# Performance work log

Measured on AMD Instinct MI355X. Metric: run time of the kernel, lower is better.

The kernel has to match this reference:

```python
import jax, jax.numpy as jnp
import numpy as np

N = 50000      # nodes
E = 800000     # edges (avg degree 16)
F_IN = 256     # num_node_features
H = 256        # hidden_dim
L = 2          # num_message_passing_rounds - 1 hidden conv layers


def setup_inputs() -> dict:
    key = jax.random.key(0)
    ks = jax.random.split(key, 8)
    x = jax.random.normal(ks[0], (N, F_IN), dtype=jnp.float32)
    edge_index = jax.random.randint(ks[1], (2, E), 0, N, dtype=jnp.int32)
    init = lambda k, shape, fan: jax.random.normal(k, shape, dtype=jnp.float32) / np.float32(np.sqrt(fan))
    WA_in = init(ks[2], (F_IN, H), F_IN)   # proj_in.A weight (stored [in,out])
    WB_in = init(ks[3], (F_IN, H), F_IN)   # proj_in.B weight
    A_stack = init(ks[4], (L, H, H), H)    # conv layers' A weights
    B_stack = init(ks[5], (L, H, H), H)    # conv layers' B weights
    W_out = init(ks[6], (H, 1), H)         # proj_out weight
    b_out = jnp.zeros((1,), jnp.float32)   # proj_out bias
    return {"x": x, "edge_index": edge_index, "WA_in": WA_in, "WB_in": WB_in,
            "A_stack": A_stack, "B_stack": B_stack, "W_out": W_out, "b_out": b_out}


def reference(x, edge_index, WA_in, WB_in, A_stack, B_stack, W_out, b_out):
    src, dst = edge_index[0], edge_index[1]
    # in-degree per node; PyG scatter-mean divides by max(deg, 1)
    deg = jax.ops.segment_sum(jnp.ones((E,), x.dtype), dst, num_segments=N)
    inv_deg = (1.0 / jnp.maximum(deg, 1.0))[:, None]  # [N,1]

    def mean_agg(h):
        # gather x_j = h[src], scatter-mean into dst -> [N, d]
        return jax.ops.segment_sum(h[src], dst, num_segments=N) * inv_deg

    # proj_in: A(mean_msg) + B(x)
    h = mean_agg(x) @ WA_in + x @ WB_in
    # hidden conv rounds with sigmoid (use_relu=False)
    for i in range(L):
        h = jax.nn.sigmoid(mean_agg(h) @ A_stack[i] + h @ B_stack[i])
    # proj_out + squeeze (output_logits=True)
    return (h @ W_out + b_out).squeeze()  # [N]
```

## Files before the change

### kernel.cpp

```cpp
#include <hip/hip_runtime.h>

typedef unsigned short u16;
typedef unsigned int u32;
typedef __attribute__((ext_vector_type(8))) short short8;
typedef __attribute__((ext_vector_type(4))) float f32x4;
typedef __attribute__((ext_vector_type(2))) float f32x2;

__device__ __forceinline__ float bf2f(u16 u) {
    return __uint_as_float(((u32)u) << 16);
}
__device__ __forceinline__ u16 f2bf(float f) {
    u32 u = __float_as_uint(f);
    u += 0x7fff + ((u >> 16) & 1);
    return (u16)(u >> 16);
}
__device__ __forceinline__ u32 pack2(float a, float b) {
    return (u32)f2bf(a) | ((u32)f2bf(b) << 16);
}
__device__ __forceinline__ u32 pk_fp8x4(float f0, float f1, float f2, float f3) {
    int w = __builtin_amdgcn_cvt_pk_fp8_f32(f0, f1, 0, false);
    w = __builtin_amdgcn_cvt_pk_fp8_f32(f2, f3, w, true);
    return (u32)w;
}
__device__ __forceinline__ void acc4(float* a, u32 w) {
    f32x2 lo = __builtin_amdgcn_cvt_pk_f32_fp8((int)w, false);
    f32x2 hi = __builtin_amdgcn_cvt_pk_f32_fp8((int)w, true);
    a[0] += lo.x; a[1] += lo.y; a[2] += hi.x; a[3] += hi.y;
}
__device__ __forceinline__ void acc4m(float* a, u32 w, float m) {
    f32x2 lo = __builtin_amdgcn_cvt_pk_f32_fp8((int)w, false);
    f32x2 hi = __builtin_amdgcn_cvt_pk_f32_fp8((int)w, true);
    a[0] += m * lo.x; a[1] += m * lo.y; a[2] += m * hi.x; a[3] += m * hi.y;
}
__device__ __forceinline__ void acc16(float* a, uint4 v) {
    acc4(a + 0, v.x); acc4(a + 4, v.y); acc4(a + 8, v.z); acc4(a + 12, v.w);
}
__device__ __forceinline__ void acc16m(float* a, uint4 v, float m) {
    acc4m(a + 0, v.x, m); acc4m(a + 4, v.y, m); acc4m(a + 8, v.z, m); acc4m(a + 12, v.w, m);
}


__global__ void cvt_x_kernel(const float* __restrict__ x, u16* __restrict__ xb,
                             u32* __restrict__ xq, int n) {
    int i = blockIdx.x * 256 + threadIdx.x;
    int row = i >> 6;
    ushort4 o;
    u32 q;
    if (row < n) {
        float4 v = ((const float4*)x)[i];
        o.x = f2bf(v.x); o.y = f2bf(v.y); o.z = f2bf(v.z); o.w = f2bf(v.w);
        q = pk_fp8x4(v.x, v.y, v.z, v.w);
    } else {
        o.x = o.y = o.z = o.w = 0;
        q = 0;
    }
    ((ushort4*)xb)[i] = o;
    xq[i] = q;
}

__global__ void cvt_h_kernel(const u16* __restrict__ hb, uint2* __restrict__ hq, int ngroups) {
    int j = blockIdx.x * 256 + threadIdx.x;
    if (j >= ngroups) return;
    uint4 v = ((const uint4*)hb)[j];
    float f0 = bf2f(v.x & 0xffff), f1 = bf2f(v.x >> 16);
    float f2 = bf2f(v.y & 0xffff), f3 = bf2f(v.y >> 16);
    float f4 = bf2f(v.z & 0xffff), f5 = bf2f(v.z >> 16);
    float f6 = bf2f(v.w & 0xffff), f7 = bf2f(v.w >> 16);
    uint2 o;
    o.x = pk_fp8x4(f0, f1, f2, f3);
    o.y = pk_fp8x4(f4, f5, f6, f7);
    hq[j] = o;
}

__global__ void cvt_w_kernel(const float* __restrict__ WA, const float* __restrict__ WB,
                             const float* __restrict__ As, const float* __restrict__ Bs,
                             u16* __restrict__ wT, int nlayers) {
    int i = blockIdx.x * 256 + threadIdx.x;
    const int per = 256 * 512;
    if (i >= nlayers * per) return;
    int l = i / per;
    int rem = i - l * per;
    int nn = rem >> 9;
    int k = rem & 511;
    const float* Aw = (l == 0) ? WA : As + (size_t)(l - 1) * 65536;
    const float* Bw = (l == 0) ? WB : Bs + (size_t)(l - 1) * 65536;
    float v = (k < 256) ? Aw[(size_t)k * 256 + nn] : Bw[(size_t)(k - 256) * 256 + nn];
    wT[i] = f2bf(v);
}


__global__ void count_kernel(const int* __restrict__ dst, int* __restrict__ deg, int e) {
    int i = blockIdx.x * 256 + threadIdx.x;
    if (i < e) atomicAdd(&deg[dst[i]], 1);
}

__global__ void scan_local_kernel(const int* __restrict__ deg, int* __restrict__ rowptr,
                                  int* __restrict__ bsum, int n) {
    __shared__ int sh[256];
    int t = threadIdx.x;
    int i = blockIdx.x * 256 + t;
    int v = (i < n) ? deg[i] : 0;
    int x = v;
    sh[t] = x; __syncthreads();
    for (int o = 1; o < 256; o <<= 1) {
        int y = (t >= o) ? sh[t - o] : 0;
        __syncthreads();
        x += y; sh[t] = x; __syncthreads();
    }
    if (i < n) rowptr[i] = x - v;
    if (t == 255) bsum[blockIdx.x] = x;
}

__global__ void scan_block_kernel(const int* __restrict__ bsum, int* __restrict__ boff, int nb) {
    __shared__ int sh[256];
    int t = threadIdx.x;
    int v = (t < nb) ? bsum[t] : 0;
    int x = v;
    sh[t] = x; __syncthreads();
    for (int o = 1; o < 256; o <<= 1) {
        int y = (t >= o) ? sh[t - o] : 0;
        __syncthreads();
        x += y; sh[t] = x; __syncthreads();
    }
    if (t < nb) boff[t] = x - v;
}

__global__ void scan_add_kernel(int* __restrict__ rowptr, const int* __restrict__ boff,
                                const int* __restrict__ deg, float* __restrict__ invd,
                                int n, int e) {
    int i = blockIdx.x * 256 + threadIdx.x;
    if (i < n) {
        rowptr[i] += boff[i >> 8];
        int d = deg[i];
        invd[i] = 1.0f / (float)(d > 0 ? d : 1);
    }
    if (i == 0) rowptr[n] = e;
}

__global__ void fill_kernel(const int* __restrict__ src, const int* __restrict__ dst,
                            const int* __restrict__ rowptr, int* __restrict__ fillc,
                            int* __restrict__ srcs, int e) {
    int i = blockIdx.x * 256 + threadIdx.x;
    if (i >= e) return;
    int d = dst[i];
    int pos = rowptr[d] + atomicAdd(&fillc[d], 1);
    srcs[pos] = src[i];
}


__global__ __launch_bounds__(256) void agg_kernel(const unsigned char* __restrict__ q,
                                                  u16* __restrict__ mb,
                                                  const int* __restrict__ rowptr,
                                                  const int* __restrict__ srcs,
                                                  const float* __restrict__ invd,
                                                  int n, int npad) {
    int gw = (blockIdx.x * 256 + threadIdx.x) >> 6;
    int lane = threadIdx.x & 63;
    int qd = lane >> 4;
    int fl = lane & 15;
    if (gw >= npad) return;
    u16* orow = mb + (size_t)gw * 256;
    if (gw >= n) {
        if (lane < 16) {
            uint4 z; z.x = z.y = z.z = z.w = 0;
            uint4* p = (uint4*)(orow + lane * 16);
            p[0] = z; p[1] = z;
        }
        return;
    }
    int beg = rowptr[gw], end = rowptr[gw + 1];
    float a[16];
#pragma unroll
    for (int i = 0; i < 16; ++i) a[i] = 0.f;
    for (int base = beg; base < end; base += 64) {
        int cnt = end - base;
        if (cnt > 64) cnt = 64;
        int el = (lane < cnt) ? srcs[base + lane] : 0;
        int t = 0;
        for (; 4 * t + 8 <= cnt; t += 2) {
            int s0 = __shfl(el, 4 * t + qd);
            int s1 = __shfl(el, 4 * t + 4 + qd);
            uint4 v0 = *(const uint4*)(q + (size_t)s0 * 256 + fl * 16);
            uint4 v1 = *(const uint4*)(q + (size_t)s1 * 256 + fl * 16);
            acc16(a, v0);
            acc16(a, v1);
        }
        for (; 4 * t < cnt; ++t) {
            int ei = 4 * t + qd;
            int sj = __shfl(el, ei & 63);
            float m = (ei < cnt) ? 1.0f : 0.0f;
            uint4 v = *(const uint4*)(q + (size_t)sj * 256 + fl * 16);
            acc16m(a, v, m);
        }
    }
#pragma unroll
    for (int i = 0; i < 16; ++i) {
        a[i] += __shfl_xor(a[i], 16);
        a[i] += __shfl_xor(a[i], 32);
    }
    if (lane < 16) {
        float sc = invd[gw];
        uint4 o0, o1;
        o0.x = pack2(a[0] * sc, a[1] * sc);
        o0.y = pack2(a[2] * sc, a[3] * sc);
        o0.z = pack2(a[4] * sc, a[5] * sc);
        o0.w = pack2(a[6] * sc, a[7] * sc);
        o1.x = pack2(a[8] * sc, a[9] * sc);
        o1.y = pack2(a[10] * sc, a[11] * sc);
        o1.z = pack2(a[12] * sc, a[13] * sc);
        o1.w = pack2(a[14] * sc, a[15] * sc);
        uint4* p = (uint4*)(orow + lane * 16);
        p[0] = o0; p[1] = o1;
    }
}


__global__ __launch_bounds__(256, 2) void gemm_kernel(const u16* __restrict__ mA,
                                                      const u16* __restrict__ cur,
                                                      const u16* __restrict__ wT,
                                                      u16* __restrict__ outb,
                                                      const float* __restrict__ wo,
                                                      const float* __restrict__ bo,
                                                      float* __restrict__ out,
                                                      int n, int apply_sigmoid, int fin) {
    __shared__ u16 lA[128 * 32];
    __shared__ u16 lB[256 * 32];
    __shared__ float lO[2][128];
    int r0 = blockIdx.x * 128;
    int tid = threadIdx.x;
    int lane = tid & 63;
    int w = tid >> 6;
    int wrow = w >> 1, wcol = w & 1;
    int lrow = lane & 15, quad = lane >> 4;

    f32x4 acc[4][8] = {};

    for (int ks = 0; ks < 16; ++ks) {
        int k0 = ks * 32;
        const u16* srcA = (k0 < 256) ? mA : cur;
        int kk = k0 & 255;
        __syncthreads();
#pragma unroll
        for (int p = 0; p < 2; ++p) {
            int li = p * 256 + tid;
            int row = li >> 2;
            int seg = (li & 3) << 3;
            const u16* gA = srcA + (size_t)(r0 + row) * 256 + kk + seg;
            __builtin_amdgcn_global_load_lds(
                (__attribute__((address_space(1))) u32*)(gA),
                (__attribute__((address_space(3))) u32*)(lA + (size_t)li * 8), 16, 0, 0);
        }
#pragma unroll
        for (int p = 0; p < 4; ++p) {
            int li = p * 256 + tid;
            int row = li >> 2;
            int seg = (li & 3) << 3;
            const u16* gB = wT + (size_t)row * 512 + k0 + seg;
            __builtin_amdgcn_global_load_lds(
                (__attribute__((address_space(1))) u32*)(gB),
                (__attribute__((address_space(3))) u32*)(lB + (size_t)li * 8), 16, 0, 0);
        }
        __syncthreads();

        short8 a[4], b[8];
#pragma unroll
        for (int t = 0; t < 4; ++t)
            a[t] = *(const short8*)(lA + ((size_t)(wrow * 64 + t * 16 + lrow) * 32 + quad * 8));
#pragma unroll
        for (int t = 0; t < 8; ++t)
            b[t] = *(const short8*)(lB + ((size_t)(wcol * 128 + t * 16 + lrow) * 32 + quad * 8));
#pragma unroll
        for (int rt = 0; rt < 4; ++rt)
#pragma unroll
            for (int ct = 0; ct < 8; ++ct)
                acc[rt][ct] = __builtin_amdgcn_mfma_f32_16x16x32_bf16(a[rt], b[ct], acc[rt][ct], 0, 0, 0);
    }

    if (!fin) {
#pragma unroll
        for (int rt = 0; rt < 4; ++rt) {
            int rbase = r0 + wrow * 64 + rt * 16 + quad * 4;
#pragma unroll
            for (int r = 0; r < 4; ++r) {
                int row = rbase + r;
                if (row < n) {
#pragma unroll
                    for (int ct = 0; ct < 8; ++ct) {
                        float v = acc[rt][ct][r];
                        if (apply_sigmoid) v = 1.0f / (1.0f + __expf(-v));
                        outb[(size_t)row * 256 + wcol * 128 + ct * 16 + lrow] = f2bf(v);
                    }
                }
            }
        }
    } else {
        float wv[8];
#pragma unroll
        for (int ct = 0; ct < 8; ++ct) wv[ct] = wo[wcol * 128 + ct * 16 + lrow];
#pragma unroll
        for (int rt = 0; rt < 4; ++rt) {
#pragma unroll
            for (int r = 0; r < 4; ++r) {
                float s = 0.f;
#pragma unroll
                for (int ct = 0; ct < 8; ++ct) {
                    float v = acc[rt][ct][r];
                    v = 1.0f / (1.0f + __expf(-v));
                    s += v * wv[ct];
                }
                s += __shfl_xor(s, 1);
                s += __shfl_xor(s, 2);
                s += __shfl_xor(s, 4);
                s += __shfl_xor(s, 8);
                if (lrow == 0) {
                    int rowlocal = wrow * 64 + rt * 16 + quad * 4 + r;
                    lO[wcol][rowlocal] = s;
                }
            }
        }
        __syncthreads();
        if (tid < 128) {
            int row = r0 + tid;
            if (row < n) out[row] = lO[0][tid] + lO[1][tid] + bo[0];
        }
    }
}


extern "C" void kernel_launch(void* const* d_in, const int* in_sizes, int n_in,
                              void* d_out, int out_size, void* d_ws, size_t ws_size,
                              hipStream_t stream) {
    const float* x  = (const float*)d_in[0];
    const int*   ei = (const int*)d_in[1];
    const float* WA = (const float*)d_in[2];
    const float* WB = (const float*)d_in[3];
    const float* As = (const float*)d_in[4];
    const float* Bs = (const float*)d_in[5];
    const float* Wo = (const float*)d_in[6];
    const float* bo = (const float*)d_in[7];
    float* out = (float*)d_out;

    const int H = 256;
    int N = in_sizes[0] / H;
    int E = in_sizes[1] / 2;
    int L = in_sizes[4] / (H * H);
    int NPAD = (N + 127) & ~127;
    int nb = (N + 255) / 256;

    char* wsp = (char*)d_ws;
    size_t off = 0;
    auto alloc = [&](size_t b) { size_t o = off; off += (b + 255) & ~(size_t)255; return o; };
    int*   rowptr = (int*)(wsp + alloc((size_t)(NPAD + 1) * 4));
    int*   deg    = (int*)(wsp + alloc((size_t)N * 4));
    int*   fillc  = (int*)(wsp + alloc((size_t)N * 4));
    int*   bsum   = (int*)(wsp + alloc(1024));
    int*   boff   = (int*)(wsp + alloc(1024));
    float* invd   = (float*)(wsp + alloc((size_t)NPAD * 4));
    int*   srcs   = (int*)(wsp + alloc((size_t)E * 4));
    u16*   xb     = (u16*)(wsp + alloc((size_t)NPAD * H * 2));
    u16*   hbuf   = (u16*)(wsp + alloc((size_t)NPAD * H * 2));
    u16*   mb     = (u16*)(wsp + alloc((size_t)NPAD * H * 2));
    u32*   xq     = (u32*)(wsp + alloc((size_t)NPAD * H));
    uint2* hq     = (uint2*)(wsp + alloc((size_t)NPAD * H));
    u16*   wT     = (u16*)(wsp + alloc((size_t)(L + 1) * 512 * 256 * 2));

    const int* esrc = ei;
    const int* edst = ei + E;

    hipMemsetAsync(deg, 0, (size_t)N * 4, stream);
    hipMemsetAsync(fillc, 0, (size_t)N * 4, stream);

    cvt_x_kernel<<<NPAD / 4, 256, 0, stream>>>(x, xb, xq, N);
    cvt_w_kernel<<<((L + 1) * 512 * 256 + 255) / 256, 256, 0, stream>>>(WA, WB, As, Bs, wT, L + 1);
    count_kernel<<<(E + 255) / 256, 256, 0, stream>>>(edst, deg, E);
    scan_local_kernel<<<nb, 256, 0, stream>>>(deg, rowptr, bsum, N);
    scan_block_kernel<<<1, 256, 0, stream>>>(bsum, boff, nb);
    scan_add_kernel<<<nb, 256, 0, stream>>>(rowptr, boff, deg, invd, N, E);
    fill_kernel<<<(E + 255) / 256, 256, 0, stream>>>(esrc, edst, rowptr, fillc, srcs, E);

    const u16* cur = xb;
    const unsigned char* curq = (const unsigned char*)xq;
    for (int s = 0; s <= L; ++s) {
        int fin = (s == L) ? 1 : 0;
        agg_kernel<<<NPAD / 4, 256, 0, stream>>>(curq, mb, rowptr, srcs, invd, N, NPAD);
        gemm_kernel<<<NPAD / 128, 256, 0, stream>>>(mb, cur, wT + (size_t)s * 512 * 256, hbuf,
                                                    Wo, bo, out, N, s > 0 ? 1 : 0, fin);
        if (!fin) {
            cvt_h_kernel<<<(N * 32 + 255) / 256, 256, 0, stream>>>(hbuf, hq, N * 32);
            cur = hbuf;
            curq = (const unsigned char*)hq;
        }
    }
}
```

Measured before the change: 392.4 us.

## Build CSR with two-pass shared-memory bucketed radix sort instead of global atomics

New measurement: 341.8 us. 1.15x faster.

```diff
diff --git a/kernel.cpp b/kernel.cpp
--- a/kernel.cpp
+++ b/kernel.cpp
@@ -89,17 +89,32 @@
 }
 
 
-__global__ void count_kernel(const int* __restrict__ dst, int* __restrict__ deg, int e) {
-    int i = blockIdx.x * 256 + threadIdx.x;
-    if (i < e) atomicAdd(&deg[dst[i]], 1);
-}
-
-__global__ void scan_local_kernel(const int* __restrict__ deg, int* __restrict__ rowptr,
-                                  int* __restrict__ bsum, int n) {
+__global__ __launch_bounds__(256) void hist_kernel(const int* __restrict__ dst,
+                                                   int* __restrict__ ccnt, int e, int nb) {
+    __shared__ int h[256];
+    int tid = threadIdx.x;
+    h[tid] = 0;
+    __syncthreads();
+    int e0 = blockIdx.x * 4096;
+#pragma unroll
+    for (int j = 0; j < 16; ++j) {
+        int i = e0 + j * 256 + tid;
+        if (i < e) atomicAdd(&h[dst[i] >> 8], 1);
+    }
+    __syncthreads();
+    if (tid < nb) {
+        int v = h[tid];
+        if (v) atomicAdd(&ccnt[tid], v);
+    }
+}
+
+__global__ __launch_bounds__(256) void scan_coarse_kernel(const int* __restrict__ ccnt,
+                                                          int* __restrict__ cbase,
+                                                          int* __restrict__ rowptr,
+                                                          int nb, int n, int e) {
     __shared__ int sh[256];
     int t = threadIdx.x;
-    int i = blockIdx.x * 256 + t;
-    int v = (i < n) ? deg[i] : 0;
+    int v = (t < nb) ? ccnt[t] : 0;
     int x = v;
     sh[t] = x; __syncthreads();
     for (int o = 1; o < 256; o <<= 1) {
@@ -107,44 +122,84 @@
         __syncthreads();
         x += y; sh[t] = x; __syncthreads();
     }
-    if (i < n) rowptr[i] = x - v;
-    if (t == 255) bsum[blockIdx.x] = x;
-}
-
-__global__ void scan_block_kernel(const int* __restrict__ bsum, int* __restrict__ boff, int nb) {
-    __shared__ int sh[256];
-    int t = threadIdx.x;
-    int v = (t < nb) ? bsum[t] : 0;
-    int x = v;
-    sh[t] = x; __syncthreads();
+    if (t < nb) cbase[t] = x - v;
+    if (t == 0) { cbase[nb] = e; rowptr[n] = e; }
+}
+
+__global__ __launch_bounds__(256) void passA_kernel(const int* __restrict__ src,
+                                                    const int* __restrict__ dst,
+                                                    const int* __restrict__ cbase,
+                                                    int* __restrict__ cfill,
+                                                    u32* __restrict__ tmp, int e, int nb) {
+    __shared__ int ph[256], pb[256], pr[256], cb[256];
+    __shared__ u32 ed[4096];
+    int tid = threadIdx.x;
+    ph[tid] = 0; pr[tid] = 0;
+    cb[tid] = (tid < nb) ? cbase[tid] : 0;
+    __syncthreads();
+    int e0 = blockIdx.x * 4096;
+#pragma unroll
+    for (int j = 0; j < 16; ++j) {
+        int i = e0 + j * 256 + tid;
+        u32 p = 0xFFFFFFFFu;
+        if (i < e) {
+            int d = dst[i];
+            p = ((u32)d << 16) | (u32)src[i];
+            atomicAdd(&ph[d >> 8], 1);
+        }
+        ed[j * 256 + tid] = p;
+    }
+    __syncthreads();
+    pb[tid] = (tid < nb && ph[tid]) ? atomicAdd(&cfill[tid], ph[tid]) : 0;
+    __syncthreads();
+#pragma unroll
+    for (int j = 0; j < 16; ++j) {
+        u32 p = ed[j * 256 + tid];
+        if (p != 0xFFFFFFFFu) {
+            int bk = p >> 24;
+            int r = atomicAdd(&pr[bk], 1);
+            tmp[cb[bk] + pb[bk] + r] = p;
+        }
+    }
+}
+
+__global__ __launch_bounds__(256) void passB_kernel(const u32* __restrict__ tmp,
+                                                    const int* __restrict__ cbase,
+                                                    int* __restrict__ rowptr,
+                                                    float* __restrict__ invd,
+                                                    int* __restrict__ srcs, int n) {
+    __shared__ int h[256], loc[256], cnt2[256], sh[256];
+    int b = blockIdx.x;
+    int tid = threadIdx.x;
+    int base = cbase[b];
+    int cnt = cbase[b + 1] - base;
+    int node0 = b << 8;
+    h[tid] = 0; cnt2[tid] = 0;
+    __syncthreads();
+    for (int i = tid; i < cnt; i += 256)
+        atomicAdd(&h[(tmp[base + i] >> 16) & 255], 1);
+    __syncthreads();
+    int c = h[tid];
+    int x = c;
+    sh[tid] = x; __syncthreads();
     for (int o = 1; o < 256; o <<= 1) {
-        int y = (t >= o) ? sh[t - o] : 0;
+        int y = (tid >= o) ? sh[tid - o] : 0;
         __syncthreads();
-        x += y; sh[t] = x; __syncthreads();
-    }
-    if (t < nb) boff[t] = x - v;
-}
-
-__global__ void scan_add_kernel(int* __restrict__ rowptr, const int* __restrict__ boff,
-                                const int* __restrict__ deg, float* __restrict__ invd,
-                                int n, int e) {
-    int i = blockIdx.x * 256 + threadIdx.x;
-    if (i < n) {
-        rowptr[i] += boff[i >> 8];
-        int d = deg[i];
-        invd[i] = 1.0f / (float)(d > 0 ? d : 1);
-    }
-    if (i == 0) rowptr[n] = e;
-}
-
-__global__ void fill_kernel(const int* __restrict__ src, const int* __restrict__ dst,
-                            const int* __restrict__ rowptr, int* __restrict__ fillc,
-                            int* __restrict__ srcs, int e) {
-    int i = blockIdx.x * 256 + threadIdx.x;
-    if (i >= e) return;
-    int d = dst[i];
-    int pos = rowptr[d] + atomicAdd(&fillc[d], 1);
-    srcs[pos] = src[i];
+        x += y; sh[tid] = x; __syncthreads();
+    }
+    loc[tid] = x - c;
+    int node = node0 + tid;
+    if (node < n) {
+        rowptr[node] = base + x - c;
+        invd[node] = 1.0f / (float)(c > 0 ? c : 1);
+    }
+    __syncthreads();
+    for (int i = tid; i < cnt; i += 256) {
+        u32 p = tmp[base + i];
+        int ln = (p >> 16) & 255;
+        int r = atomicAdd(&cnt2[ln], 1);
+        srcs[base + loc[ln] + r] = (int)(p & 0xffffu);
+    }
 }
 
 
@@ -345,16 +400,15 @@
     int E = in_sizes[1] / 2;
     int L = in_sizes[4] / (H * H);
     int NPAD = (N + 127) & ~127;
-    int nb = (N + 255) / 256;
+    int NB = (N + 255) >> 8;
 
     char* wsp = (char*)d_ws;
     size_t off = 0;
     auto alloc = [&](size_t b) { size_t o = off; off += (b + 255) & ~(size_t)255; return o; };
     int*   rowptr = (int*)(wsp + alloc((size_t)(NPAD + 1) * 4));
-    int*   deg    = (int*)(wsp + alloc((size_t)N * 4));
-    int*   fillc  = (int*)(wsp + alloc((size_t)N * 4));
-    int*   bsum   = (int*)(wsp + alloc(1024));
-    int*   boff   = (int*)(wsp + alloc(1024));
+    int*   ccnt   = (int*)(wsp + alloc(1024));
+    int*   cbase  = (int*)(wsp + alloc(1032 + 256));
+    int*   cfill  = (int*)(wsp + alloc(1024));
     float* invd   = (float*)(wsp + alloc((size_t)NPAD * 4));
     int*   srcs   = (int*)(wsp + alloc((size_t)E * 4));
     u16*   xb     = (u16*)(wsp + alloc((size_t)NPAD * H * 2));
@@ -363,20 +417,21 @@
     u32*   xq     = (u32*)(wsp + alloc((size_t)NPAD * H));
     uint2* hq     = (uint2*)(wsp + alloc((size_t)NPAD * H));
     u16*   wT     = (u16*)(wsp + alloc((size_t)(L + 1) * 512 * 256 * 2));
+    u32*   tmp    = (u32*)mb;
 
     const int* esrc = ei;
     const int* edst = ei + E;
 
-    hipMemsetAsync(deg, 0, (size_t)N * 4, stream);
-    hipMemsetAsync(fillc, 0, (size_t)N * 4, stream);
-
+    hipMemsetAsync(ccnt, 0, 1024, stream);
+    hipMemsetAsync(cfill, 0, 1024, stream);
+
+    int gridE = (E + 4095) / 4096;
     cvt_x_kernel<<<NPAD / 4, 256, 0, stream>>>(x, xb, xq, N);
     cvt_w_kernel<<<((L + 1) * 512 * 256 + 255) / 256, 256, 0, stream>>>(WA, WB, As, Bs, wT, L + 1);
-    count_kernel<<<(E + 255) / 256, 256, 0, stream>>>(edst, deg, E);
-    scan_local_kernel<<<nb, 256, 0, stream>>>(deg, rowptr, bsum, N);
-    scan_block_kernel<<<1, 256, 0, stream>>>(bsum, boff, nb);
-    scan_add_kernel<<<nb, 256, 0, stream>>>(rowptr, boff, deg, invd, N, E);
-    fill_kernel<<<(E + 255) / 256, 256, 0, stream>>>(esrc, edst, rowptr, fillc, srcs, E);
+    hist_kernel<<<gridE, 256, 0, stream>>>(edst, ccnt, E, NB);
+    scan_coarse_kernel<<<1, 256, 0, stream>>>(ccnt, cbase, rowptr, NB, N, E);
+    passA_kernel<<<gridE, 256, 0, stream>>>(esrc, edst, cbase, cfill, tmp, E, NB);
+    passB_kernel<<<NB, 256, 0, stream>>>(tmp, cbase, rowptr, invd, srcs, N);
 
     const u16* cur = xb;
     const unsigned char* curq = (const unsigned char*)xq;
```
